# Kernel optimization log

Hardware: AMD Instinct MI355X
Metric: run time of the kernel (lower is better)

## Reference

```python
import jax, jax.numpy as jnp
import numpy as np


def setup_inputs() -> dict:
    key = jax.random.key(0)
    ks = jax.random.split(key, 5)
    B, H, S, D = 4, 16, 2048, 64
    queries = jax.random.normal(ks[0], (B, H, S, D), dtype=jnp.float32)
    keys = jax.random.normal(ks[1], (B, H, S, D), dtype=jnp.float32)
    values = jax.random.normal(ks[2], (B, H, S, D), dtype=jnp.float32)
    W_out = jax.random.normal(ks[3], (D, D), dtype=jnp.float32) / np.sqrt(D)
    b_out = jax.random.normal(ks[4], (D,), dtype=jnp.float32) * 0.01
    return {"queries": queries, "keys": keys, "values": values, "W_out": W_out, "b_out": b_out}


def reference(queries, keys, values, W_out, b_out):
    # scores: [B,H,S,S] = Q K^T / sqrt(D)
    scale = 1.0 / np.sqrt(queries.shape[-1]).astype(np.float32)
    scores = jnp.einsum("bhqd,bhkd->bhqk", queries, keys) * scale
    # concrete attention distribution: softmax over keys axis
    distr = jax.nn.softmax(scores, axis=-1)
    # weighted sum of values: [B,H,S,D]
    out = jnp.einsum("bhqk,bhkd->bhqd", distr, values)
    # out projection (nn.Linear: x @ W^T + b)
    out = jnp.einsum("bhqd,ed->bhqe", out, W_out) + b_out
    return out
```

## Files before the change

kernel.cpp:

```cpp
#include <hip/hip_runtime.h>
#include <math.h>


typedef __attribute__((ext_vector_type(8)))  short    s16x8;
typedef __attribute__((ext_vector_type(4)))  float    f32x4;
typedef __attribute__((ext_vector_type(16))) float    f32x16;
typedef __attribute__((ext_vector_type(4)))  unsigned u32x4;

#define KQSCALE 0.18033688011112042f

__device__ __forceinline__ unsigned short f2bu(float x) {
    __bf16 v = (__bf16)x;
    return __builtin_bit_cast(unsigned short, v);
}
__device__ __forceinline__ short f2b(float x) { return (short)f2bu(x); }
__device__ __forceinline__ float b2f(short s) {
    __bf16 v = __builtin_bit_cast(__bf16, (unsigned short)s);
    return (float)v;
}
__device__ __forceinline__ unsigned pack2(float lo, float hi) {
    return (unsigned)f2bu(lo) | ((unsigned)f2bu(hi) << 16);
}
__device__ __forceinline__ int swzK(int row) { return (row & 7) << 4; }
__device__ __forceinline__ int swzV(int row) { return (((row >> 4) & 3) ^ (row & 7)) << 4; }

#define PLSWAP(x, y) asm("v_permlane32_swap_b32 %0, %1" : "+v"(x), "+v"(y))

#define BARRIER()                                              \
    do {                                                       \
        asm volatile("s_waitcnt lgkmcnt(0)" ::: "memory");     \
        __builtin_amdgcn_s_barrier();                          \
    } while (0)

#define WAVE_LDS_FENCE()                                       \
    do {                                                       \
        asm volatile("s_waitcnt lgkmcnt(0)" ::: "memory");     \
        __builtin_amdgcn_sched_barrier(0);                     \
    } while (0)

#define QK2(SA, SB, KsC, KT)                                                    \
    f32x16 SA = {}; f32x16 SB = {};                                             \
    __builtin_amdgcn_s_setprio(1);                                              \
    _Pragma("unroll")                                                           \
    for (int dt = 0; dt < 4; ++dt) {                                            \
        const int krow = (KT) * 32 + q32;                                       \
        s16x8 kf = *(s16x8*)((KsC) + krow * 128 +                               \
                             ((dt * 32 + h * 16) ^ swzK(krow)));                \
        SA = __builtin_amdgcn_mfma_f32_32x32x16_bf16(kf, qfA[dt], SA, 0, 0, 0); \
        SB = __builtin_amdgcn_mfma_f32_32x32x16_bf16(kf, qfB[dt], SB, 0, 0, 0); \
    }                                                                           \
    __builtin_amdgcn_s_setprio(0);

#define PVQ2(SA, SB, VtC, KT, T)                                               \
    do {                                                                       \
        const float ea0 = __builtin_amdgcn_exp2f((SA)[8 * (T) + 0]);           \
        const float ea1 = __builtin_amdgcn_exp2f((SA)[8 * (T) + 1]);           \
        const float ea2 = __builtin_amdgcn_exp2f((SA)[8 * (T) + 2]);           \
        const float ea3 = __builtin_amdgcn_exp2f((SA)[8 * (T) + 3]);           \
        const float ea4 = __builtin_amdgcn_exp2f((SA)[8 * (T) + 4]);           \
        const float ea5 = __builtin_amdgcn_exp2f((SA)[8 * (T) + 5]);           \
        const float ea6 = __builtin_amdgcn_exp2f((SA)[8 * (T) + 6]);           \
        const float ea7 = __builtin_amdgcn_exp2f((SA)[8 * (T) + 7]);           \
        const float eb0 = __builtin_amdgcn_exp2f((SB)[8 * (T) + 0]);           \
        const float eb1 = __builtin_amdgcn_exp2f((SB)[8 * (T) + 1]);           \
        const float eb2 = __builtin_amdgcn_exp2f((SB)[8 * (T) + 2]);           \
        const float eb3 = __builtin_amdgcn_exp2f((SB)[8 * (T) + 3]);           \
        const float eb4 = __builtin_amdgcn_exp2f((SB)[8 * (T) + 4]);           \
        const float eb5 = __builtin_amdgcn_exp2f((SB)[8 * (T) + 5]);           \
        const float eb6 = __builtin_amdgcn_exp2f((SB)[8 * (T) + 6]);           \
        const float eb7 = __builtin_amdgcn_exp2f((SB)[8 * (T) + 7]);           \
        unsigned ka0 = pack2(ea0, ea1), ka1 = pack2(ea2, ea3);                 \
        unsigned ka2 = pack2(ea4, ea5), ka3 = pack2(ea6, ea7);                 \
        PLSWAP(ka0, ka2);                                                      \
        PLSWAP(ka1, ka3);                                                      \
        u32x4 pwA; pwA[0] = ka0; pwA[1] = ka1; pwA[2] = ka2; pwA[3] = ka3;     \
        const s16x8 pA_ = __builtin_bit_cast(s16x8, pwA);                      \
        unsigned kb0 = pack2(eb0, eb1), kb1 = pack2(eb2, eb3);                 \
        unsigned kb2 = pack2(eb4, eb5), kb3 = pack2(eb6, eb7);                 \
        PLSWAP(kb0, kb2);                                                      \
        PLSWAP(kb1, kb3);                                                      \
        u32x4 pwB; pwB[0] = kb0; pwB[1] = kb1; pwB[2] = kb2; pwB[3] = kb3;     \
        const s16x8 pB_ = __builtin_bit_cast(s16x8, pwB);                      \
        const int kbo = (KT) * 64 + (T) * 32 + h * 16;                         \
        __builtin_amdgcn_s_setprio(1);                                         \
        s16x8 vf0 = *(s16x8*)((VtC) + q32 * 128 + (kbo ^ swzV(q32)));          \
        s16x8 vf1 = *(s16x8*)((VtC) + (32 + q32) * 128 + (kbo ^ swzV(32 + q32))); \
        accA0 = __builtin_amdgcn_mfma_f32_32x32x16_bf16(pA_, vf0, accA0, 0, 0, 0); \
        accB0 = __builtin_amdgcn_mfma_f32_32x32x16_bf16(pB_, vf0, accB0, 0, 0, 0); \
        accA1 = __builtin_amdgcn_mfma_f32_32x32x16_bf16(pA_, vf1, accA1, 0, 0, 0); \
        accB1 = __builtin_amdgcn_mfma_f32_32x32x16_bf16(pB_, vf1, accB1, 0, 0, 0); \
        rsA = __builtin_amdgcn_mfma_f32_32x32x16_bf16(pA_, onesV, rsA, 0, 0, 0); \
        rsB = __builtin_amdgcn_mfma_f32_32x32x16_bf16(pB_, onesV, rsB, 0, 0, 0); \
        __builtin_amdgcn_s_setprio(0);                                         \
    } while (0)

__global__ __launch_bounds__(512) void attn_fused(
    const float* __restrict__ Qg, const float* __restrict__ Kg,
    const float* __restrict__ Vg, const float* __restrict__ Wg,
    const float* __restrict__ bg, float* __restrict__ outg)
{
    __shared__ __align__(16) char smem[65536];
    char* Ks0 = smem;
    char* Vt0 = smem + 8192;
    char* Ks1 = smem + 16384;
    char* Vt1 = smem + 24576;

    const int tid  = threadIdx.x;
    const int wave = tid >> 6;
    const int lane = tid & 63;
    const int h    = lane >> 5;
    const int q32  = lane & 31;
    const int g    = lane >> 4;
    const int c    = lane & 15;

    const int orig = blockIdx.x;
    const int wg   = (orig & 7) * 32 + (orig >> 3);
    const int bh   = wg >> 2;
    const int qblk = wg & 3;

    const float* Qh = Qg + (size_t)bh * (2048 * 64);
    const float* Kh = Kg + (size_t)bh * (2048 * 64);
    const float* Vh = Vg + (size_t)bh * (2048 * 64);
    float*       Oh = outg + (size_t)bh * (2048 * 64);

    const int qbaseA = qblk * 512 + wave * 32;
    const int qbaseB = qbaseA + 256;

    const int srow = tid >> 3;
    const int scb  = (tid & 7) * 8;
    const int vk   = (tid >> 4) * 2;
    const int vd4  = (tid & 15) * 4;
    const int kOff = srow * 64 + scb;
    const int vOff = vk * 64 + vd4;

    f32x4 qLa[4], qLb[4], qLc[4], qLd[4];
#pragma unroll
    for (int dt = 0; dt < 4; ++dt) {
        const float* sA = Qh + (size_t)(qbaseA + q32) * 64 + dt * 16 + h * 8;
        const float* sB = Qh + (size_t)(qbaseB + q32) * 64 + dt * 16 + h * 8;
        qLa[dt] = *(const f32x4*)(sA);
        qLb[dt] = *(const f32x4*)(sA + 4);
        qLc[dt] = *(const f32x4*)(sB);
        qLd[dt] = *(const f32x4*)(sB + 4);
    }

    f32x4 rK0, rK1;
    f32x4 rV0, rV1;

    auto issueK = [&](int chunk) {
        const float* p = Kh + (size_t)chunk * 4096 + kOff;
        rK0 = *(const f32x4*)(p);
        rK1 = *(const f32x4*)(p + 4);
    };
    auto issueV = [&](int chunk) {
        const float* p = Vh + (size_t)chunk * 4096 + vOff;
        rV0 = *(const f32x4*)(p);
        rV1 = *(const f32x4*)(p + 64);
    };
    auto stageK = [&](char* KsD) {
        u32x4 wA;
        wA[0] = pack2(rK0[0], rK0[1]); wA[1] = pack2(rK0[2], rK0[3]);
        wA[2] = pack2(rK1[0], rK1[1]); wA[3] = pack2(rK1[2], rK1[3]);
        *(u32x4*)(KsD + srow * 128 + ((scb * 2) ^ swzK(srow))) = wA;
    };
    auto stageV = [&](char* VtD) {
#pragma unroll
        for (int i = 0; i < 4; ++i) {
            const int d = vd4 + i;
            *(unsigned*)(VtD + d * 128 + ((2 * vk) ^ swzV(d))) = pack2(rV0[i], rV1[i]);
        }
    };

    s16x8 qfA[4], qfB[4];
#pragma unroll
    for (int dt = 0; dt < 4; ++dt) {
        u32x4 fA, fB;
        fA[0] = pack2(qLa[dt][0] * KQSCALE, qLa[dt][1] * KQSCALE);
        fA[1] = pack2(qLa[dt][2] * KQSCALE, qLa[dt][3] * KQSCALE);
        fA[2] = pack2(qLb[dt][0] * KQSCALE, qLb[dt][1] * KQSCALE);
        fA[3] = pack2(qLb[dt][2] * KQSCALE, qLb[dt][3] * KQSCALE);
        fB[0] = pack2(qLc[dt][0] * KQSCALE, qLc[dt][1] * KQSCALE);
        fB[1] = pack2(qLc[dt][2] * KQSCALE, qLc[dt][3] * KQSCALE);
        fB[2] = pack2(qLd[dt][0] * KQSCALE, qLd[dt][1] * KQSCALE);
        fB[3] = pack2(qLd[dt][2] * KQSCALE, qLd[dt][3] * KQSCALE);
        qfA[dt] = __builtin_bit_cast(s16x8, fA);
        qfB[dt] = __builtin_bit_cast(s16x8, fB);
    }

    f32x16 accA0 = {}, accA1 = {}, accB0 = {}, accB1 = {};
    f32x16 rsA = {}, rsB = {};
    u32x4 onesW;
    onesW[0] = 0x3F803F80u; onesW[1] = 0x3F803F80u;
    onesW[2] = 0x3F803F80u; onesW[3] = 0x3F803F80u;
    const s16x8 onesV = __builtin_bit_cast(s16x8, onesW);

    auto one_iter = [&](char* KsC, char* VtC, char* KsN, char* VtN, int kc) {
        QK2(s0A, s0B, KsC, 0);
        PVQ2(s0A, s0B, VtC, 0, 0);
        if (kc < 31) {
            stageK(KsN);
            if (kc < 30) issueK(kc + 2);
        }
        PVQ2(s0A, s0B, VtC, 0, 1);
        QK2(s1A, s1B, KsC, 1);
        PVQ2(s1A, s1B, VtC, 1, 0);
        if (kc < 31) {
            stageV(VtN);
            if (kc < 30) issueV(kc + 2);
        }
        PVQ2(s1A, s1B, VtC, 1, 1);
        BARRIER();
    };

    issueK(0);
    issueV(0);
    stageK(Ks0);
    stageV(Vt0);
    issueK(1);
    issueV(1);
    BARRIER();

    for (int kc = 0; kc < 32; kc += 2) {
        one_iter(Ks0, Vt0, Ks1, Vt1, kc);
        one_iter(Ks1, Vt1, Ks0, Vt0, kc + 1);
    }

#pragma unroll
    for (int r = 0; r < 16; ++r) {
        const float ivA = __builtin_amdgcn_rcpf(rsA[r]);
        const float ivB = __builtin_amdgcn_rcpf(rsB[r]);
        accA0[r] *= ivA;  accA1[r] *= ivA;
        accB0[r] *= ivB;  accB1[r] *= ivB;
    }

    auto stageO = [&](const f32x16& a0, const f32x16& a1) {
        char* Ow = smem + wave * 8192;
#pragma unroll
        for (int r = 0; r < 16; ++r) {
            const int row = (r & 3) + 8 * (r >> 2) + 4 * h;
            const int sw  = (row & 7) << 5;
            *(float*)(Ow + row * 256 + ((q32 * 4)       ^ sw)) = a0[r];
            *(float*)(Ow + row * 256 + ((128 + q32 * 4) ^ sw)) = a1[r];
        }
    };
    auto project = [&](int qb) {
        char* Ow = smem + wave * 8192;
        f32x4 po[2][4];
#pragma unroll
        for (int rt = 0; rt < 2; ++rt)
#pragma unroll
            for (int et = 0; et < 4; ++et) {
                po[rt][et][0] = 0.f; po[rt][et][1] = 0.f;
                po[rt][et][2] = 0.f; po[rt][et][3] = 0.f;
            }
#pragma unroll
        for (int kh = 0; kh < 2; ++kh) {
            s16x8 ahi[2], alo[2];
#pragma unroll
            for (int rt = 0; rt < 2; ++rt) {
                const int row = rt * 16 + c;
                const int rb  = row * 256;
                const int rsw = (row & 7) << 5;
                const int o0  = (kh * 128 + g * 32) ^ rsw;
                f32x4 x0 = *(f32x4*)(Ow + rb + o0);
                f32x4 x1 = *(f32x4*)(Ow + rb + o0 + 16);
                s16x8 hh8, lo8;
#pragma unroll
                for (int j = 0; j < 4; ++j) {
                    const short hv = f2b(x0[j]);
                    hh8[j] = hv;  lo8[j] = f2b(x0[j] - b2f(hv));
                }
#pragma unroll
                for (int j = 0; j < 4; ++j) {
                    const short hv = f2b(x1[j]);
                    hh8[4 + j] = hv;  lo8[4 + j] = f2b(x1[j] - b2f(hv));
                }
                ahi[rt] = hh8; alo[rt] = lo8;
            }
#pragma unroll
            for (int et = 0; et < 4; ++et) {
                const float* ws = Wg + (et * 16 + c) * 64 + kh * 32 + g * 8;
                f32x4 w0 = *(const f32x4*)ws;
                f32x4 w1 = *(const f32x4*)(ws + 4);
                s16x8 whi, wlo;
#pragma unroll
                for (int j = 0; j < 4; ++j) {
                    const short hv = f2b(w0[j]);
                    whi[j] = hv;  wlo[j] = f2b(w0[j] - b2f(hv));
                }
#pragma unroll
                for (int j = 0; j < 4; ++j) {
                    const short hv = f2b(w1[j]);
                    whi[4 + j] = hv;  wlo[4 + j] = f2b(w1[j] - b2f(hv));
                }
#pragma unroll
                for (int rt = 0; rt < 2; ++rt) {
                    po[rt][et] = __builtin_amdgcn_mfma_f32_16x16x32_bf16(ahi[rt], whi, po[rt][et], 0, 0, 0);
                    po[rt][et] = __builtin_amdgcn_mfma_f32_16x16x32_bf16(alo[rt], whi, po[rt][et], 0, 0, 0);
                    po[rt][et] = __builtin_amdgcn_mfma_f32_16x16x32_bf16(ahi[rt], wlo, po[rt][et], 0, 0, 0);
                }
            }
        }
#pragma unroll
        for (int et = 0; et < 4; ++et) {
            const float bb = bg[et * 16 + c];
#pragma unroll
            for (int rt = 0; rt < 2; ++rt)
#pragma unroll
                for (int r = 0; r < 4; ++r) {
                    const int qrow = qb + rt * 16 + 4 * g + r;
                    Oh[(size_t)qrow * 64 + et * 16 + c] = po[rt][et][r] + bb;
                }
        }
    };

    BARRIER();
    stageO(accA0, accA1);
    WAVE_LDS_FENCE();
    project(qbaseA);
    WAVE_LDS_FENCE();
    stageO(accB0, accB1);
    WAVE_LDS_FENCE();
    project(qbaseB);
}

extern "C" void kernel_launch(void* const* d_in, const int* in_sizes, int n_in,
                              void* d_out, int out_size, void* d_ws, size_t ws_size,
                              hipStream_t stream) {
    const float* Q = (const float*)d_in[0];
    const float* K = (const float*)d_in[1];
    const float* V = (const float*)d_in[2];
    const float* W = (const float*)d_in[3];
    const float* b = (const float*)d_in[4];
    float* out = (float*)d_out;
    hipLaunchKernelGGL(attn_fused, dim3(256), dim3(512), 0, stream, Q, K, V, W, b, out);
}
```

Baseline: 96.06 us.

## Halve per-wave query tiles and double workgroup count to 512

Each wave now handles one 32-row query tile instead of two, so each workgroup covers 256 queries and the grid doubles to 512 blocks. This lowers register pressure and gives more blocks than the 256 CUs, which could improve occupancy and load balance. The cost is that K/V tiles are loaded and staged from global memory twice as often per head, and each K/V LDS fragment is reused across half as many MFMAs.

```diff
diff --git a/kernel.cpp b/kernel.cpp
--- a/kernel.cpp
+++ b/kernel.cpp
@@ -38,59 +38,41 @@
         __builtin_amdgcn_sched_barrier(0);                     \
     } while (0)
 
-#define QK2(SA, SB, KsC, KT)                                                    \
-    f32x16 SA = {}; f32x16 SB = {};                                             \
+#define QK1(SVAR, KsC, KT)                                                      \
+    f32x16 SVAR = {};                                                           \
     __builtin_amdgcn_s_setprio(1);                                              \
     _Pragma("unroll")                                                           \
     for (int dt = 0; dt < 4; ++dt) {                                            \
         const int krow = (KT) * 32 + q32;                                       \
         s16x8 kf = *(s16x8*)((KsC) + krow * 128 +                               \
                              ((dt * 32 + h * 16) ^ swzK(krow)));                \
-        SA = __builtin_amdgcn_mfma_f32_32x32x16_bf16(kf, qfA[dt], SA, 0, 0, 0); \
-        SB = __builtin_amdgcn_mfma_f32_32x32x16_bf16(kf, qfB[dt], SB, 0, 0, 0); \
+        SVAR = __builtin_amdgcn_mfma_f32_32x32x16_bf16(kf, qf[dt], SVAR, 0, 0, 0); \
     }                                                                           \
     __builtin_amdgcn_s_setprio(0);
 
-#define PVQ2(SA, SB, VtC, KT, T)                                               \
+#define PVQ1(S, VtC, KT, T)                                                    \
     do {                                                                       \
-        const float ea0 = __builtin_amdgcn_exp2f((SA)[8 * (T) + 0]);           \
-        const float ea1 = __builtin_amdgcn_exp2f((SA)[8 * (T) + 1]);           \
-        const float ea2 = __builtin_amdgcn_exp2f((SA)[8 * (T) + 2]);           \
-        const float ea3 = __builtin_amdgcn_exp2f((SA)[8 * (T) + 3]);           \
-        const float ea4 = __builtin_amdgcn_exp2f((SA)[8 * (T) + 4]);           \
-        const float ea5 = __builtin_amdgcn_exp2f((SA)[8 * (T) + 5]);           \
-        const float ea6 = __builtin_amdgcn_exp2f((SA)[8 * (T) + 6]);           \
-        const float ea7 = __builtin_amdgcn_exp2f((SA)[8 * (T) + 7]);           \
-        const float eb0 = __builtin_amdgcn_exp2f((SB)[8 * (T) + 0]);           \
-        const float eb1 = __builtin_amdgcn_exp2f((SB)[8 * (T) + 1]);           \
-        const float eb2 = __builtin_amdgcn_exp2f((SB)[8 * (T) + 2]);           \
-        const float eb3 = __builtin_amdgcn_exp2f((SB)[8 * (T) + 3]);           \
-        const float eb4 = __builtin_amdgcn_exp2f((SB)[8 * (T) + 4]);           \
-        const float eb5 = __builtin_amdgcn_exp2f((SB)[8 * (T) + 5]);           \
-        const float eb6 = __builtin_amdgcn_exp2f((SB)[8 * (T) + 6]);           \
-        const float eb7 = __builtin_amdgcn_exp2f((SB)[8 * (T) + 7]);           \
-        unsigned ka0 = pack2(ea0, ea1), ka1 = pack2(ea2, ea3);                 \
-        unsigned ka2 = pack2(ea4, ea5), ka3 = pack2(ea6, ea7);                 \
-        PLSWAP(ka0, ka2);                                                      \
-        PLSWAP(ka1, ka3);                                                      \
-        u32x4 pwA; pwA[0] = ka0; pwA[1] = ka1; pwA[2] = ka2; pwA[3] = ka3;     \
-        const s16x8 pA_ = __builtin_bit_cast(s16x8, pwA);                      \
-        unsigned kb0 = pack2(eb0, eb1), kb1 = pack2(eb2, eb3);                 \
-        unsigned kb2 = pack2(eb4, eb5), kb3 = pack2(eb6, eb7);                 \
-        PLSWAP(kb0, kb2);                                                      \
-        PLSWAP(kb1, kb3);                                                      \
-        u32x4 pwB; pwB[0] = kb0; pwB[1] = kb1; pwB[2] = kb2; pwB[3] = kb3;     \
-        const s16x8 pB_ = __builtin_bit_cast(s16x8, pwB);                      \
+        const float e0 = __builtin_amdgcn_exp2f((S)[8 * (T) + 0]);             \
+        const float e1 = __builtin_amdgcn_exp2f((S)[8 * (T) + 1]);             \
+        const float e2 = __builtin_amdgcn_exp2f((S)[8 * (T) + 2]);             \
+        const float e3 = __builtin_amdgcn_exp2f((S)[8 * (T) + 3]);             \
+        const float e4 = __builtin_amdgcn_exp2f((S)[8 * (T) + 4]);             \
+        const float e5 = __builtin_amdgcn_exp2f((S)[8 * (T) + 5]);             \
+        const float e6 = __builtin_amdgcn_exp2f((S)[8 * (T) + 6]);             \
+        const float e7 = __builtin_amdgcn_exp2f((S)[8 * (T) + 7]);             \
+        unsigned k0 = pack2(e0, e1), k1 = pack2(e2, e3);                       \
+        unsigned k2 = pack2(e4, e5), k3 = pack2(e6, e7);                       \
+        PLSWAP(k0, k2);                                                        \
+        PLSWAP(k1, k3);                                                        \
+        u32x4 pw; pw[0] = k0; pw[1] = k1; pw[2] = k2; pw[3] = k3;              \
+        const s16x8 pa = __builtin_bit_cast(s16x8, pw);                        \
         const int kbo = (KT) * 64 + (T) * 32 + h * 16;                         \
         __builtin_amdgcn_s_setprio(1);                                         \
         s16x8 vf0 = *(s16x8*)((VtC) + q32 * 128 + (kbo ^ swzV(q32)));          \
         s16x8 vf1 = *(s16x8*)((VtC) + (32 + q32) * 128 + (kbo ^ swzV(32 + q32))); \
-        accA0 = __builtin_amdgcn_mfma_f32_32x32x16_bf16(pA_, vf0, accA0, 0, 0, 0); \
-        accB0 = __builtin_amdgcn_mfma_f32_32x32x16_bf16(pB_, vf0, accB0, 0, 0, 0); \
-        accA1 = __builtin_amdgcn_mfma_f32_32x32x16_bf16(pA_, vf1, accA1, 0, 0, 0); \
-        accB1 = __builtin_amdgcn_mfma_f32_32x32x16_bf16(pB_, vf1, accB1, 0, 0, 0); \
-        rsA = __builtin_amdgcn_mfma_f32_32x32x16_bf16(pA_, onesV, rsA, 0, 0, 0); \
-        rsB = __builtin_amdgcn_mfma_f32_32x32x16_bf16(pB_, onesV, rsB, 0, 0, 0); \
+        acc0 = __builtin_amdgcn_mfma_f32_32x32x16_bf16(pa, vf0, acc0, 0, 0, 0); \
+        acc1 = __builtin_amdgcn_mfma_f32_32x32x16_bf16(pa, vf1, acc1, 0, 0, 0); \
+        rs   = __builtin_amdgcn_mfma_f32_32x32x16_bf16(pa, onesV, rs, 0, 0, 0); \
         __builtin_amdgcn_s_setprio(0);                                         \
     } while (0)
 
@@ -114,17 +96,16 @@
     const int c    = lane & 15;
 
     const int orig = blockIdx.x;
-    const int wg   = (orig & 7) * 32 + (orig >> 3);
-    const int bh   = wg >> 2;
-    const int qblk = wg & 3;
+    const int wg   = (orig & 7) * 64 + (orig >> 3);
+    const int bh   = wg >> 3;
+    const int qblk = wg & 7;
 
     const float* Qh = Qg + (size_t)bh * (2048 * 64);
     const float* Kh = Kg + (size_t)bh * (2048 * 64);
     const float* Vh = Vg + (size_t)bh * (2048 * 64);
     float*       Oh = outg + (size_t)bh * (2048 * 64);
 
-    const int qbaseA = qblk * 512 + wave * 32;
-    const int qbaseB = qbaseA + 256;
+    const int qbase = qblk * 256 + wave * 32;
 
     const int srow = tid >> 3;
     const int scb  = (tid & 7) * 8;
@@ -133,15 +114,12 @@
     const int kOff = srow * 64 + scb;
     const int vOff = vk * 64 + vd4;
 
-    f32x4 qLa[4], qLb[4], qLc[4], qLd[4];
+    f32x4 qLa[4], qLb[4];
 #pragma unroll
     for (int dt = 0; dt < 4; ++dt) {
-        const float* sA = Qh + (size_t)(qbaseA + q32) * 64 + dt * 16 + h * 8;
-        const float* sB = Qh + (size_t)(qbaseB + q32) * 64 + dt * 16 + h * 8;
+        const float* sA = Qh + (size_t)(qbase + q32) * 64 + dt * 16 + h * 8;
         qLa[dt] = *(const f32x4*)(sA);
         qLb[dt] = *(const f32x4*)(sA + 4);
-        qLc[dt] = *(const f32x4*)(sB);
-        qLd[dt] = *(const f32x4*)(sB + 4);
     }
 
     f32x4 rK0, rK1;
@@ -171,44 +149,39 @@
         }
     };
 
-    s16x8 qfA[4], qfB[4];
+    s16x8 qf[4];
 #pragma unroll
     for (int dt = 0; dt < 4; ++dt) {
-        u32x4 fA, fB;
-        fA[0] = pack2(qLa[dt][0] * KQSCALE, qLa[dt][1] * KQSCALE);
-        fA[1] = pack2(qLa[dt][2] * KQSCALE, qLa[dt][3] * KQSCALE);
-        fA[2] = pack2(qLb[dt][0] * KQSCALE, qLb[dt][1] * KQSCALE);
-        fA[3] = pack2(qLb[dt][2] * KQSCALE, qLb[dt][3] * KQSCALE);
-        fB[0] = pack2(qLc[dt][0] * KQSCALE, qLc[dt][1] * KQSCALE);
-        fB[1] = pack2(qLc[dt][2] * KQSCALE, qLc[dt][3] * KQSCALE);
-        fB[2] = pack2(qLd[dt][0] * KQSCALE, qLd[dt][1] * KQSCALE);
-        fB[3] = pack2(qLd[dt][2] * KQSCALE, qLd[dt][3] * KQSCALE);
-        qfA[dt] = __builtin_bit_cast(s16x8, fA);
-        qfB[dt] = __builtin_bit_cast(s16x8, fB);
-    }
-
-    f32x16 accA0 = {}, accA1 = {}, accB0 = {}, accB1 = {};
-    f32x16 rsA = {}, rsB = {};
+        u32x4 f;
+        f[0] = pack2(qLa[dt][0] * KQSCALE, qLa[dt][1] * KQSCALE);
+        f[1] = pack2(qLa[dt][2] * KQSCALE, qLa[dt][3] * KQSCALE);
+        f[2] = pack2(qLb[dt][0] * KQSCALE, qLb[dt][1] * KQSCALE);
+        f[3] = pack2(qLb[dt][2] * KQSCALE, qLb[dt][3] * KQSCALE);
+        qf[dt] = __builtin_bit_cast(s16x8, f);
+    }
+
+    f32x16 acc0 = {}, acc1 = {};
+    f32x16 rs = {};
     u32x4 onesW;
     onesW[0] = 0x3F803F80u; onesW[1] = 0x3F803F80u;
     onesW[2] = 0x3F803F80u; onesW[3] = 0x3F803F80u;
     const s16x8 onesV = __builtin_bit_cast(s16x8, onesW);
 
     auto one_iter = [&](char* KsC, char* VtC, char* KsN, char* VtN, int kc) {
-        QK2(s0A, s0B, KsC, 0);
-        PVQ2(s0A, s0B, VtC, 0, 0);
+        QK1(s0, KsC, 0);
+        PVQ1(s0, VtC, 0, 0);
         if (kc < 31) {
             stageK(KsN);
             if (kc < 30) issueK(kc + 2);
         }
-        PVQ2(s0A, s0B, VtC, 0, 1);
-        QK2(s1A, s1B, KsC, 1);
-        PVQ2(s1A, s1B, VtC, 1, 0);
+        PVQ1(s0, VtC, 0, 1);
+        QK1(s1, KsC, 1);
+        PVQ1(s1, VtC, 1, 0);
         if (kc < 31) {
             stageV(VtN);
             if (kc < 30) issueV(kc + 2);
         }
-        PVQ2(s1A, s1B, VtC, 1, 1);
+        PVQ1(s1, VtC, 1, 1);
         BARRIER();
     };
 
@@ -227,101 +200,92 @@
 
 #pragma unroll
     for (int r = 0; r < 16; ++r) {
-        const float ivA = __builtin_amdgcn_rcpf(rsA[r]);
-        const float ivB = __builtin_amdgcn_rcpf(rsB[r]);
-        accA0[r] *= ivA;  accA1[r] *= ivA;
-        accB0[r] *= ivB;  accB1[r] *= ivB;
-    }
-
-    auto stageO = [&](const f32x16& a0, const f32x16& a1) {
-        char* Ow = smem + wave * 8192;
-#pragma unroll
-        for (int r = 0; r < 16; ++r) {
-            const int row = (r & 3) + 8 * (r >> 2) + 4 * h;
-            const int sw  = (row & 7) << 5;
-            *(float*)(Ow + row * 256 + ((q32 * 4)       ^ sw)) = a0[r];
-            *(float*)(Ow + row * 256 + ((128 + q32 * 4) ^ sw)) = a1[r];
-        }
-    };
-    auto project = [&](int qb) {
-        char* Ow = smem + wave * 8192;
-        f32x4 po[2][4];
+        const float iv = __builtin_amdgcn_rcpf(rs[r]);
+        acc0[r] *= iv;
+        acc1[r] *= iv;
+    }
+
+    char* Ow = smem + wave * 8192;
+
+    BARRIER();
+#pragma unroll
+    for (int r = 0; r < 16; ++r) {
+        const int row = (r & 3) + 8 * (r >> 2) + 4 * h;
+        const int sw  = (row & 7) << 5;
+        *(float*)(Ow + row * 256 + ((q32 * 4)       ^ sw)) = acc0[r];
+        *(float*)(Ow + row * 256 + ((128 + q32 * 4) ^ sw)) = acc1[r];
+    }
+    WAVE_LDS_FENCE();
+
+    f32x4 po[2][4];
+#pragma unroll
+    for (int rt = 0; rt < 2; ++rt)
+#pragma unroll
+        for (int et = 0; et < 4; ++et) {
+            po[rt][et][0] = 0.f; po[rt][et][1] = 0.f;
+            po[rt][et][2] = 0.f; po[rt][et][3] = 0.f;
+        }
+
+#pragma unroll
+    for (int kh = 0; kh < 2; ++kh) {
+        s16x8 ahi[2], alo[2];
+#pragma unroll
+        for (int rt = 0; rt < 2; ++rt) {
+            const int row = rt * 16 + c;
+            const int rb  = row * 256;
+            const int rsw = (row & 7) << 5;
+            const int o0  = (kh * 128 + g * 32) ^ rsw;
+            f32x4 x0 = *(f32x4*)(Ow + rb + o0);
+            f32x4 x1 = *(f32x4*)(Ow + rb + o0 + 16);
+            s16x8 hh8, lo8;
+#pragma unroll
+            for (int j = 0; j < 4; ++j) {
+                const short hv = f2b(x0[j]);
+                hh8[j] = hv;  lo8[j] = f2b(x0[j] - b2f(hv));
+            }
+#pragma unroll
+            for (int j = 0; j < 4; ++j) {
+                const short hv = f2b(x1[j]);
+                hh8[4 + j] = hv;  lo8[4 + j] = f2b(x1[j] - b2f(hv));
+            }
+            ahi[rt] = hh8; alo[rt] = lo8;
+        }
+#pragma unroll
+        for (int et = 0; et < 4; ++et) {
+            const float* ws = Wg + (et * 16 + c) * 64 + kh * 32 + g * 8;
+            f32x4 w0 = *(const f32x4*)ws;
+            f32x4 w1 = *(const f32x4*)(ws + 4);
+            s16x8 whi, wlo;
+#pragma unroll
+            for (int j = 0; j < 4; ++j) {
+                const short hv = f2b(w0[j]);
+                whi[j] = hv;  wlo[j] = f2b(w0[j] - b2f(hv));
+            }
+#pragma unroll
+            for (int j = 0; j < 4; ++j) {
+                const short hv = f2b(w1[j]);
+                whi[4 + j] = hv;  wlo[4 + j] = f2b(w1[j] - b2f(hv));
+            }
+#pragma unroll
+            for (int rt = 0; rt < 2; ++rt) {
+                po[rt][et] = __builtin_amdgcn_mfma_f32_16x16x32_bf16(ahi[rt], whi, po[rt][et], 0, 0, 0);
+                po[rt][et] = __builtin_amdgcn_mfma_f32_16x16x32_bf16(alo[rt], whi, po[rt][et], 0, 0, 0);
+                po[rt][et] = __builtin_amdgcn_mfma_f32_16x16x32_bf16(ahi[rt], wlo, po[rt][et], 0, 0, 0);
+            }
+        }
+    }
+
+#pragma unroll
+    for (int et = 0; et < 4; ++et) {
+        const float bb = bg[et * 16 + c];
 #pragma unroll
         for (int rt = 0; rt < 2; ++rt)
 #pragma unroll
-            for (int et = 0; et < 4; ++et) {
-                po[rt][et][0] = 0.f; po[rt][et][1] = 0.f;
-                po[rt][et][2] = 0.f; po[rt][et][3] = 0.f;
-            }
-#pragma unroll
-        for (int kh = 0; kh < 2; ++kh) {
-            s16x8 ahi[2], alo[2];
-#pragma unroll
-            for (int rt = 0; rt < 2; ++rt) {
-                const int row = rt * 16 + c;
-                const int rb  = row * 256;
-                const int rsw = (row & 7) << 5;
-                const int o0  = (kh * 128 + g * 32) ^ rsw;
-                f32x4 x0 = *(f32x4*)(Ow + rb + o0);
-                f32x4 x1 = *(f32x4*)(Ow + rb + o0 + 16);
-                s16x8 hh8, lo8;
-#pragma unroll
-                for (int j = 0; j < 4; ++j) {
-                    const short hv = f2b(x0[j]);
-                    hh8[j] = hv;  lo8[j] = f2b(x0[j] - b2f(hv));
-                }
-#pragma unroll
-                for (int j = 0; j < 4; ++j) {
-                    const short hv = f2b(x1[j]);
-                    hh8[4 + j] = hv;  lo8[4 + j] = f2b(x1[j] - b2f(hv));
-                }
-                ahi[rt] = hh8; alo[rt] = lo8;
-            }
-#pragma unroll
-            for (int et = 0; et < 4; ++et) {
-                const float* ws = Wg + (et * 16 + c) * 64 + kh * 32 + g * 8;
-                f32x4 w0 = *(const f32x4*)ws;
-                f32x4 w1 = *(const f32x4*)(ws + 4);
-                s16x8 whi, wlo;
-#pragma unroll
-                for (int j = 0; j < 4; ++j) {
-                    const short hv = f2b(w0[j]);
-                    whi[j] = hv;  wlo[j] = f2b(w0[j] - b2f(hv));
-                }
-#pragma unroll
-                for (int j = 0; j < 4; ++j) {
-                    const short hv = f2b(w1[j]);
-                    whi[4 + j] = hv;  wlo[4 + j] = f2b(w1[j] - b2f(hv));
-                }
-#pragma unroll
-                for (int rt = 0; rt < 2; ++rt) {
-                    po[rt][et] = __builtin_amdgcn_mfma_f32_16x16x32_bf16(ahi[rt], whi, po[rt][et], 0, 0, 0);
-                    po[rt][et] = __builtin_amdgcn_mfma_f32_16x16x32_bf16(alo[rt], whi, po[rt][et], 0, 0, 0);
-                    po[rt][et] = __builtin_amdgcn_mfma_f32_16x16x32_bf16(ahi[rt], wlo, po[rt][et], 0, 0, 0);
-                }
-            }
-        }
-#pragma unroll
-        for (int et = 0; et < 4; ++et) {
-            const float bb = bg[et * 16 + c];
-#pragma unroll
-            for (int rt = 0; rt < 2; ++rt)
-#pragma unroll
-                for (int r = 0; r < 4; ++r) {
-                    const int qrow = qb + rt * 16 + 4 * g + r;
-                    Oh[(size_t)qrow * 64 + et * 16 + c] = po[rt][et][r] + bb;
-                }
-        }
-    };
-
-    BARRIER();
-    stageO(accA0, accA1);
-    WAVE_LDS_FENCE();
-    project(qbaseA);
-    WAVE_LDS_FENCE();
-    stageO(accB0, accB1);
-    WAVE_LDS_FENCE();
-    project(qbaseB);
+            for (int r = 0; r < 4; ++r) {
+                const int qrow = qbase + rt * 16 + 4 * g + r;
+                Oh[(size_t)qrow * 64 + et * 16 + c] = po[rt][et][r] + bb;
+            }
+    }
 }
 
 extern "C" void kernel_launch(void* const* d_in, const int* in_sizes, int n_in,
@@ -333,5 +297,5 @@
     const float* W = (const float*)d_in[3];
     const float* b = (const float*)d_in[4];
     float* out = (float*)d_out;
-    hipLaunchKernelGGL(attn_fused, dim3(256), dim3(512), 0, stream, Q, K, V, W, b, out);
-}
+    hipLaunchKernelGGL(attn_fused, dim3(512), dim3(512), 0, stream, Q, K, V, W, b, out);
+}
```

After: 113.1 us. 17.7% more time.

## Quad-buffer K/V LDS tiles and barrier once per two chunks

Applied to the files above, without the earlier changes.

Expands the K/V shared-memory ring from two to four buffers, using the already-allocated 64KB. Each iteration now stages the chunk two ahead and issues global loads three ahead. This lets the workgroup barrier run once per two key chunks instead of every chunk. The aim is to cut synchronization stalls and give loads more latency slack, at the cost of more complex buffer indexing and deeper prefetch bookkeeping.

```diff
diff --git a/kernel.cpp b/kernel.cpp
--- a/kernel.cpp
+++ b/kernel.cpp
@@ -100,10 +100,14 @@
     const float* __restrict__ bg, float* __restrict__ outg)
 {
     __shared__ __align__(16) char smem[65536];
-    char* Ks0 = smem;
-    char* Vt0 = smem + 8192;
-    char* Ks1 = smem + 16384;
-    char* Vt1 = smem + 24576;
+    char* KsB0 = smem;
+    char* VtB0 = smem + 8192;
+    char* KsB1 = smem + 16384;
+    char* VtB1 = smem + 24576;
+    char* KsB2 = smem + 32768;
+    char* VtB2 = smem + 40960;
+    char* KsB3 = smem + 49152;
+    char* VtB3 = smem + 57344;
 
     const int tid  = threadIdx.x;
     const int wave = tid >> 6;
@@ -194,35 +198,37 @@
     onesW[2] = 0x3F803F80u; onesW[3] = 0x3F803F80u;
     const s16x8 onesV = __builtin_bit_cast(s16x8, onesW);
 
-    auto one_iter = [&](char* KsC, char* VtC, char* KsN, char* VtN, int kc) {
+    auto one_iter = [&](char* KsC, char* VtC, char* KsS, char* VtS, int kc) {
         QK2(s0A, s0B, KsC, 0);
         PVQ2(s0A, s0B, VtC, 0, 0);
-        if (kc < 31) {
-            stageK(KsN);
-            if (kc < 30) issueK(kc + 2);
+        if (kc <= 29) {
+            stageK(KsS);
+            if (kc <= 28) issueK(kc + 3);
         }
         PVQ2(s0A, s0B, VtC, 0, 1);
         QK2(s1A, s1B, KsC, 1);
         PVQ2(s1A, s1B, VtC, 1, 0);
-        if (kc < 31) {
-            stageV(VtN);
-            if (kc < 30) issueV(kc + 2);
+        if (kc <= 29) {
+            stageV(VtS);
+            if (kc <= 28) issueV(kc + 3);
         }
         PVQ2(s1A, s1B, VtC, 1, 1);
+    };
+
+    issueK(0); issueV(0);
+    stageK(KsB0); stageV(VtB0);
+    issueK(1); issueV(1);
+    stageK(KsB1); stageV(VtB1);
+    issueK(2); issueV(2);
+    BARRIER();
+
+    for (int kc = 0; kc < 32; kc += 4) {
+        one_iter(KsB0, VtB0, KsB2, VtB2, kc);
+        one_iter(KsB1, VtB1, KsB3, VtB3, kc + 1);
         BARRIER();
-    };
-
-    issueK(0);
-    issueV(0);
-    stageK(Ks0);
-    stageV(Vt0);
-    issueK(1);
-    issueV(1);
-    BARRIER();
-
-    for (int kc = 0; kc < 32; kc += 2) {
-        one_iter(Ks0, Vt0, Ks1, Vt1, kc);
-        one_iter(Ks1, Vt1, Ks0, Vt0, kc + 1);
+        one_iter(KsB2, VtB2, KsB0, VtB0, kc + 2);
+        one_iter(KsB3, VtB3, KsB1, VtB1, kc + 3);
+        BARRIER();
     }
 
 #pragma unroll
@@ -314,7 +320,6 @@
         }
     };
 
-    BARRIER();
     stageO(accA0, accA1);
     WAVE_LDS_FENCE();
     project(qbaseA);
```

Result: faster. 94.16 us (-2.0%).
